# Kernel tuning notes

Hardware: AMD Instinct MI355X
Metric: run time of the kernel (lower is better)

## Reference

```python
import jax, jax.numpy as jnp
import numpy as np

B, T, D, H = 64, 1024, 128, 256

def setup_inputs() -> dict:
    key = jax.random.key(0)
    ks = jax.random.split(key, 9)
    s = 1.0 / np.sqrt(H)  # torch nn.RNN init scale
    u = lambda k, shape: jax.random.uniform(k, shape, jnp.float32, -s, s)
    return {
        "x": jax.random.normal(ks[0], (B, T, D), jnp.float32),
        "W_ih0": u(ks[1], (H, D)), "W_hh0": u(ks[2], (H, H)),
        "b_ih0": u(ks[3], (H,)),   "b_hh0": u(ks[4], (H,)),
        "W_ih1": u(ks[5], (H, H)), "W_hh1": u(ks[6], (H, H)),
        "b_ih1": u(ks[7], (H,)),   "b_hh1": u(ks[8], (H,)),
    }

def _rnn_layer(x, W_ih, W_hh, b_ih, b_hh):
    # x: [B, T, Din] -> out: [B, T, H]; h_t = tanh(x_t W_ih^T + b_ih + h_{t-1} W_hh^T + b_hh)
    xW = jnp.einsum('btd,hd->bth', x, W_ih) + b_ih  # precompute input projection
    h0 = jnp.zeros((x.shape[0], W_hh.shape[0]), x.dtype)
    def step(h, xt):
        h = jnp.tanh(xt + h @ W_hh.T + b_hh)
        return h, h
    _, ys = jax.lax.scan(step, h0, jnp.swapaxes(xW, 0, 1))  # [T, B, H]
    return jnp.swapaxes(ys, 0, 1)

def reference(x, W_ih0, W_hh0, b_ih0, b_hh0, W_ih1, W_hh1, b_ih1, b_hh1):
    h = _rnn_layer(x, W_ih0, W_hh0, b_ih0, b_hh0)
    h = _rnn_layer(h, W_ih1, W_hh1, b_ih1, b_hh1)
    return jnp.transpose(h, (0, 2, 1))  # [B, H, T] per out.permute(0, 2, 1)
```

## Files before the change

### kernel.cpp

```cpp
#include <hip/hip_runtime.h>
#include <hip/hip_bf16.h>


#define B_ 64
#define T_ 1024
#define D_ 128
#define H_ 256
#define TCMAX 128

typedef _Float16 half2_t __attribute__((ext_vector_type(2)));

__device__ __forceinline__ float bf2f(unsigned short u) {
    union { unsigned int i; float f; } v;
    v.i = ((unsigned int)u) << 16;
    return v.f;
}

__device__ __forceinline__ unsigned int cvt2_bf16_to_f16(unsigned int u) {
    union { float f; unsigned int i; } a, b;
    a.i = u << 16;
    b.i = u & 0xFFFF0000u;
    union { _Float16 h[2]; unsigned int u; } r;
    r.h[0] = (_Float16)a.f;
    r.h[1] = (_Float16)b.f;
    return r.u;
}

__device__ __forceinline__ uint4 cvt8_bf16_to_f16(uint4 v) {
    uint4 r;
    r.x = cvt2_bf16_to_f16(v.x);
    r.y = cvt2_bf16_to_f16(v.y);
    r.z = cvt2_bf16_to_f16(v.z);
    r.w = cvt2_bf16_to_f16(v.w);
    return r;
}

__device__ __forceinline__ float dot2(unsigned int a, unsigned int b, float c) {
    union { unsigned int u; half2_t h; } ua, ub;
    ua.u = a; ub.u = b;
#if defined(__HIP_DEVICE_COMPILE__) && __has_builtin(__builtin_amdgcn_fdot2)
    return __builtin_amdgcn_fdot2(ua.h, ub.h, c, false);
#else
    return c + (float)ua.h.x * (float)ub.h.x + (float)ua.h.y * (float)ub.h.y;
#endif
}

__device__ __forceinline__ float fast_tanh(float x) {
#if defined(__HIP_DEVICE_COMPILE__) && __has_builtin(__builtin_amdgcn_exp2f)
    float e = __builtin_amdgcn_exp2f(x * 2.885390081777927f);
#else
    float e = __expf(2.0f * x);
#endif
#if defined(__HIP_DEVICE_COMPILE__) && __has_builtin(__builtin_amdgcn_rcpf)
    return 1.0f - 2.0f * __builtin_amdgcn_rcpf(e + 1.0f);
#else
    return 1.0f - 2.0f / (e + 1.0f);
#endif
}

__device__ __forceinline__ void lds_barrier() {
    asm volatile("s_waitcnt lgkmcnt(0)\n\ts_barrier" ::: "memory");
}

__global__ void detect_dtype(const unsigned short* __restrict__ w, int* __restrict__ flag) {
    if (threadIdx.x == 0 && blockIdx.x == 0) {
        int f = 0;
        for (int i = 0; i < 512; ++i) {
            unsigned e = (w[i] >> 7) & 0xFF;
            if (e >= 127) f = 1;
        }
        *flag = f;
    }
}

__global__ void prep_w(const void* __restrict__ wih0, const void* __restrict__ whh0,
                       const void* __restrict__ bih0, const void* __restrict__ bhh0,
                       const void* __restrict__ wih1, const void* __restrict__ whh1,
                       const void* __restrict__ bih1, const void* __restrict__ bhh1,
                       _Float16* __restrict__ owih0, _Float16* __restrict__ owhh0,
                       _Float16* __restrict__ owih1, _Float16* __restrict__ owhh1,
                       float* __restrict__ obias0, float* __restrict__ obias1,
                       uint4* __restrict__ carries, const int* __restrict__ flag) {
    const bool f32 = (*flag != 0);
    int i = blockIdx.x * 256 + threadIdx.x;
    auto rd = [&](const void* p, int idx) -> float {
        return f32 ? ((const float*)p)[idx] : bf2f(((const unsigned short*)p)[idx]);
    };
    if (i < H_ * D_) owih0[i] = (_Float16)rd(wih0, i);
    if (i < H_ * H_) {
        owhh0[i] = (_Float16)rd(whh0, i);
        owih1[i] = (_Float16)rd(wih1, i);
        owhh1[i] = (_Float16)rd(whh1, i);
    }
    if (i < H_) {
        obias0[i] = rd(bih0, i) + rd(bhh0, i);
        obias1[i] = rd(bih1, i) + rd(bhh1, i);
    }
    if (i < (2 * B_ * H_) / 8) carries[i] = uint4{0, 0, 0, 0};
}

template <int K, bool XSRC>
__device__ __forceinline__ void proj_gemm(const void* __restrict__ src,
                                          const _Float16* __restrict__ W,
                                          const float* __restrict__ bias,
                                          _Float16* __restrict__ outx,
                                          const int* __restrict__ flag,
                                          int t0, int Tc, int pb,
                                          char* __restrict__ sm, int tid) {
    constexpr int KW = K / 8;
    const int sg = tid >> 8, j = tid & 255;
    const long m0 = (long)pb * 48;
    const bool f32 = XSRC && (*flag != 0);
    uint4* xt = (uint4*)sm;

    for (int idx = tid; idx < 48 * KW; idx += 768) {
        int r = idx / KW, c = idx % KW;
        long m = m0 + r;
        uint4 v = uint4{0, 0, 0, 0};
        if (m < (long)B_ * Tc) {
            long off;
            if (XSRC) {
                long b = m / Tc, tc = m - b * Tc;
                off = (b * T_ + t0 + tc) * (long)K + (long)c * 8;
                if (f32) {
                    const float* s = (const float*)src + off;
                    union { _Float16 h[8]; uint4 u; } r8;
#pragma unroll
                    for (int q = 0; q < 8; ++q) r8.h[q] = (_Float16)s[q];
                    v = r8.u;
                } else {
                    v = cvt8_bf16_to_f16(*(const uint4*)((const unsigned short*)src + off));
                }
            } else {
                off = m * (long)K + (long)c * 8;
                v = *(const uint4*)((const _Float16*)src + off);
            }
        }
        xt[idx] = v;
    }

    uint4 w[KW];
    const uint4* wp = (const uint4*)(W + (long)j * K);
#pragma unroll
    for (int i = 0; i < KW; ++i) w[i] = wp[i];
    __syncthreads();

    const float bb = bias[j];
#pragma unroll 1
    for (int r = 0; r < 16; ++r) {
        const long m = m0 + sg * 16 + r;
        if (m < (long)B_ * Tc) {
            const uint4* xr = xt + (sg * 16 + r) * KW;
            float a0 = 0.f, a1 = 0.f, a2 = 0.f, a3 = 0.f;
#pragma unroll
            for (int i = 0; i < KW; ++i) {
                uint4 h = xr[i];
                uint4 ww = w[i];
                a0 = dot2(ww.x, h.x, a0);
                a1 = dot2(ww.y, h.y, a1);
                a2 = dot2(ww.z, h.z, a2);
                a3 = dot2(ww.w, h.w, a3);
            }
            outx[m * H_ + j] = (_Float16)(((a0 + a1) + (a2 + a3)) + bb);
        }
    }
}

__device__ __forceinline__ void scan_layer(const _Float16* __restrict__ xw,
                                           const _Float16* __restrict__ Whh,
                                           _Float16* __restrict__ carry,
                                           _Float16* __restrict__ hout,
                                           char* __restrict__ sm, int b,
                                           int tid, int Tc) {
    __builtin_amdgcn_s_setprio(1);
    _Float16* stage = (_Float16*)sm;
    _Float16* hbuf  = (_Float16*)(sm + TCMAX * H_ * 2);
    const bool act = (tid < 512);
    const int wv = tid >> 6, lane = tid & 63, half = lane >> 5;
    const int jj = (wv & 7) * 32 + (lane & 31);

    uint4 w[16];
    if (act) {
        const uint4* wp = (const uint4*)(Whh + (long)jj * H_ + half * 128);
#pragma unroll
        for (int i = 0; i < 16; ++i) w[i] = wp[i];
    }

    {
        const uint4* src = (const uint4*)(xw + (long)b * Tc * H_);
        uint4* dst = (uint4*)stage;
        for (int i = tid; i < Tc * (H_ / 8); i += 768) dst[i] = src[i];
    }
    if (tid < 256) hbuf[tid] = carry[b * H_ + tid];
    __syncthreads();

    float hlast = 0.f;
#pragma unroll 1
    for (int it = 0; it < Tc; ++it) {
        const int p = it & 1;
        if (act) {
            float xh = (float)stage[it * H_ + jj];
            const uint4* hb = (const uint4*)(hbuf + p * H_) + half * 16;
            float a0 = 0.f, a1 = 0.f, a2 = 0.f, a3 = 0.f;
#pragma unroll
            for (int i = 0; i < 16; ++i) {
                uint4 h = hb[i];
                uint4 ww = w[i];
                a0 = dot2(ww.x, h.x, a0);
                a1 = dot2(ww.y, h.y, a1);
                a2 = dot2(ww.z, h.z, a2);
                a3 = dot2(ww.w, h.w, a3);
            }
            float s = (a0 + a1) + (a2 + a3);
            s += __shfl_xor(s, 32, 64);
            float hv = fast_tanh(s + xh);
            _Float16 hf = (_Float16)hv;
            if (half == 0) hbuf[(p ^ 1) * H_ + jj] = hf;
            else           stage[it * H_ + jj]     = hf;
            hlast = hv;
        }
        lds_barrier();
    }

    if (act && half == 0) carry[b * H_ + jj] = (_Float16)hlast;
    {
        const uint4* src = (const uint4*)stage;
        uint4* dst = (uint4*)(hout + (long)b * Tc * H_);
        for (int i = tid; i < Tc * (H_ / 8); i += 768) dst[i] = src[i];
    }
}

__device__ __forceinline__ void transpose_dev(const _Float16* __restrict__ tmp,
                                              void* __restrict__ out,
                                              const int* __restrict__ flag,
                                              int t0, int Tc, int pb,
                                              char* __restrict__ sm, int tid) {
    const int nTc = (Tc + 63) >> 6;
    int bid = pb;
    const int jblk = bid & 3; bid >>= 2;
    const int tcblk = bid % nTc;
    const int b = bid / nTc;
    const bool f32o = (*flag != 0);
    float* tile = (float*)sm;
#pragma unroll
    for (int k = 0; k < 6; ++k) {
        int idx = k * 768 + tid;
        if (idx < 4096) {
            int r = idx >> 6, c = idx & 63;
            int tc = tcblk * 64 + r;
            tile[r * 65 + c] = (tc < Tc)
                ? (float)tmp[((long)b * Tc + tc) * H_ + jblk * 64 + c] : 0.f;
        }
    }
    __syncthreads();
#pragma unroll
    for (int k = 0; k < 6; ++k) {
        int idx = k * 768 + tid;
        if (idx < 4096) {
            int jr = idx >> 6, tc = idx & 63;
            if (tcblk * 64 + tc < Tc) {
                float v = tile[tc * 65 + jr];
                long o = ((long)b * H_ + jblk * 64 + jr) * (long)T_ + t0 + tcblk * 64 + tc;
                if (f32o) ((float*)out)[o] = v;
                else      ((__hip_bfloat16*)out)[o] = __float2bfloat16(v);
            }
        }
    }
}

__global__ __launch_bounds__(768, 1) void boot(
    const void* __restrict__ x, const _Float16* __restrict__ W,
    const float* __restrict__ bias, _Float16* __restrict__ outx,
    const int* __restrict__ flag, int Tc)
{
    __shared__ __align__(16) char sm[24576];
    proj_gemm<D_, true>(x, W, bias, outx, flag, 0, Tc, blockIdx.x, sm, threadIdx.x);
}

__global__ __launch_bounds__(768, 1) void mega(
    const void* __restrict__ x,
    const _Float16* __restrict__ Wih0, const _Float16* __restrict__ Whh0,
    const _Float16* __restrict__ Wih1, const _Float16* __restrict__ Whh1,
    const float* __restrict__ bias0, const float* __restrict__ bias1,
    _Float16* __restrict__ carry0, _Float16* __restrict__ carry1,
    const _Float16* __restrict__ xw0r, _Float16* __restrict__ xw0w,
    _Float16* __restrict__ h0w, const _Float16* __restrict__ h0r,
    _Float16* __restrict__ xw1w, const _Float16* __restrict__ xw1r,
    _Float16* __restrict__ h1w, const _Float16* __restrict__ h1r,
    void* __restrict__ dout, const int* __restrict__ flag,
    int v_s0, int t_p0, int v_p1, int v_s1, int t_tr, int Tc, int nproj)
{
    __shared__ __align__(16) char sm[TCMAX * H_ * 2 + 1024];
    const int bid = blockIdx.x;
    const int tid = threadIdx.x;

    if (bid < 64) {
        if (!v_s0) return;
        scan_layer(xw0r, Whh0, carry0, h0w, sm, bid, tid, Tc);
    } else if (bid < 128) {
        if (!v_s1) return;
        scan_layer(xw1r, Whh1, carry1, h1w, sm, bid - 64, tid, Tc);
    } else if (bid < 128 + nproj) {
        if (t_p0 < 0) return;
        proj_gemm<D_, true>(x, Wih0, bias0, xw0w, flag, t_p0, Tc, bid - 128, sm, tid);
    } else if (bid < 128 + 2 * nproj) {
        if (!v_p1) return;
        proj_gemm<H_, false>(h0r, Wih1, bias1, xw1w, flag, 0, Tc, bid - 128 - nproj, sm, tid);
    } else {
        if (t_tr < 0) return;
        transpose_dev(h1r, dout, flag, t_tr, Tc, bid - 128 - 2 * nproj, sm, tid);
    }
}

extern "C" void kernel_launch(void* const* d_in, const int* in_sizes, int n_in,
                              void* d_out, int out_size, void* d_ws, size_t ws_size,
                              hipStream_t stream) {
    const void* x    = d_in[0];
    const void* wih0 = d_in[1];
    const void* whh0 = d_in[2];
    const void* bih0 = d_in[3];
    const void* bhh0 = d_in[4];
    const void* wih1 = d_in[5];
    const void* whh1 = d_in[6];
    const void* bih1 = d_in[7];
    const void* bhh1 = d_in[8];
    (void)in_sizes; (void)n_in; (void)out_size;

    char* ws = (char*)d_ws;
    size_t off = 0;
    auto alloc = [&](size_t bytes) -> void* {
        void* p = ws + off;
        off += (bytes + 255) & ~(size_t)255;
        return p;
    };

    int*      flag    = (int*)alloc(256);
    _Float16* wih0_16 = (_Float16*)alloc((size_t)H_ * D_ * 2);
    _Float16* whh0_16 = (_Float16*)alloc((size_t)H_ * H_ * 2);
    _Float16* wih1_16 = (_Float16*)alloc((size_t)H_ * H_ * 2);
    _Float16* whh1_16 = (_Float16*)alloc((size_t)H_ * H_ * 2);
    float*    bias0   = (float*)alloc(H_ * 4);
    float*    bias1   = (float*)alloc(H_ * 4);
    _Float16* carry0  = (_Float16*)alloc((size_t)B_ * H_ * 2);
    _Float16* carry1  = (_Float16*)alloc((size_t)B_ * H_ * 2);

    size_t fixed = off;
    int Tc = TCMAX;
    while (Tc > 32 && fixed + 8 * ((size_t)B_ * Tc * H_ * 2 + 256) > ws_size) Tc >>= 1;
    _Float16 *xw0g[2], *xw1g[2], *h0g[2], *h1g[2];
    for (int i = 0; i < 2; ++i) xw0g[i] = (_Float16*)alloc((size_t)B_ * Tc * H_ * 2);
    for (int i = 0; i < 2; ++i) xw1g[i] = (_Float16*)alloc((size_t)B_ * Tc * H_ * 2);
    for (int i = 0; i < 2; ++i) h0g[i]  = (_Float16*)alloc((size_t)B_ * Tc * H_ * 2);
    for (int i = 0; i < 2; ++i) h1g[i]  = (_Float16*)alloc((size_t)B_ * Tc * H_ * 2);

    detect_dtype<<<1, 64, 0, stream>>>((const unsigned short*)whh0, flag);
    prep_w<<<(H_ * H_ + 255) / 256, 256, 0, stream>>>(
        wih0, whh0, bih0, bhh0, wih1, whh1, bih1, bhh1,
        wih0_16, whh0_16, wih1_16, whh1_16, bias0, bias1, (uint4*)carry0, flag);

    const int NC     = T_ / Tc;
    const int nproj  = (B_ * Tc + 47) / 48;
    const int ntrans = B_ * ((Tc + 63) / 64) * (H_ / 64);
    const int grid   = 128 + 2 * nproj + ntrans;

    boot<<<nproj, 768, 0, stream>>>(x, wih0_16, bias0, xw0g[0], flag, Tc);

    for (int d = 0; d <= NC + 2; ++d) {
        const int v_s0 = (d < NC) ? 1 : 0;
        const int t_p0 = (d + 1 < NC) ? (d + 1) * Tc : -1;
        const int v_p1 = (d - 1 >= 0 && d - 1 < NC) ? 1 : 0;
        const int v_s1 = (d - 2 >= 0 && d - 2 < NC) ? 1 : 0;
        const int t_tr = (d - 3 >= 0 && d - 3 < NC) ? (d - 3) * Tc : -1;
        mega<<<grid, 768, 0, stream>>>(
            x, wih0_16, whh0_16, wih1_16, whh1_16, bias0, bias1,
            carry0, carry1,
            xw0g[d & 1],
            xw0g[(d + 1) & 1],
            h0g[d & 1],
            h0g[(d - 1) & 1],
            xw1g[(d - 1) & 1],
            xw1g[(d - 2) & 1],
            h1g[(d - 2) & 1],
            h1g[(d - 3) & 1],
            d_out, flag, v_s0, t_p0, v_p1, v_s1, t_tr, Tc, nproj);
    }
}
```

Before: 872.0 us.

## Compute two hidden outputs per thread with 4-way K split in RNN scan

Reworks the recurrent matvec thread mapping so that each thread computes two adjacent output units over a quarter of the K dimension, instead of one unit over half of K. Each LDS load of h is reused for two weight rows, which halves h-load traffic per FLOP. The hidden-state buffer is padded into quarter-chunks with a stride of 72 to avoid bank conflicts. The reduction now needs two cross-lane shuffle stages per output, and outputs and the carry are written as packed half pairs.

```diff
diff --git a/kernel.cpp b/kernel.cpp
--- a/kernel.cpp
+++ b/kernel.cpp
@@ -7,6 +7,7 @@
 #define D_ 128
 #define H_ 256
 #define TCMAX 128
+#define HBQ 72
 
 typedef _Float16 half2_t __attribute__((ext_vector_type(2)));
 
@@ -176,14 +177,16 @@
     _Float16* stage = (_Float16*)sm;
     _Float16* hbuf  = (_Float16*)(sm + TCMAX * H_ * 2);
     const bool act = (tid < 512);
-    const int wv = tid >> 6, lane = tid & 63, half = lane >> 5;
-    const int jj = (wv & 7) * 32 + (lane & 31);
-
-    uint4 w[16];
+    const int wv = (tid >> 6) & 7, lane = tid & 63;
+    const int kq = lane >> 4;
+    const int j0 = (wv * 16 + (lane & 15)) * 2;
+
+    uint4 w0[8], w1[8];
     if (act) {
-        const uint4* wp = (const uint4*)(Whh + (long)jj * H_ + half * 128);
-#pragma unroll
-        for (int i = 0; i < 16; ++i) w[i] = wp[i];
+        const uint4* p0 = (const uint4*)(Whh + (long)j0 * H_ + kq * 64);
+        const uint4* p1 = (const uint4*)(Whh + (long)(j0 + 1) * H_ + kq * 64);
+#pragma unroll
+        for (int i = 0; i < 8; ++i) { w0[i] = p0[i]; w1[i] = p1[i]; }
     }
 
     {
@@ -191,38 +194,43 @@
         uint4* dst = (uint4*)stage;
         for (int i = tid; i < Tc * (H_ / 8); i += 768) dst[i] = src[i];
     }
-    if (tid < 256) hbuf[tid] = carry[b * H_ + tid];
+    if (tid < 256) hbuf[(tid >> 6) * HBQ + (tid & 63)] = carry[b * H_ + tid];
     __syncthreads();
 
-    float hlast = 0.f;
+    unsigned hlast = 0;
 #pragma unroll 1
     for (int it = 0; it < Tc; ++it) {
         const int p = it & 1;
         if (act) {
-            float xh = (float)stage[it * H_ + jj];
-            const uint4* hb = (const uint4*)(hbuf + p * H_) + half * 16;
-            float a0 = 0.f, a1 = 0.f, a2 = 0.f, a3 = 0.f;
-#pragma unroll
-            for (int i = 0; i < 16; ++i) {
+            const uint4* hb = (const uint4*)(hbuf + p * (4 * HBQ) + kq * HBQ);
+            float a0 = 0.f, a1 = 0.f, b0 = 0.f, b1 = 0.f;
+#pragma unroll
+            for (int i = 0; i < 8; ++i) {
                 uint4 h = hb[i];
-                uint4 ww = w[i];
-                a0 = dot2(ww.x, h.x, a0);
-                a1 = dot2(ww.y, h.y, a1);
-                a2 = dot2(ww.z, h.z, a2);
-                a3 = dot2(ww.w, h.w, a3);
-            }
-            float s = (a0 + a1) + (a2 + a3);
-            s += __shfl_xor(s, 32, 64);
-            float hv = fast_tanh(s + xh);
-            _Float16 hf = (_Float16)hv;
-            if (half == 0) hbuf[(p ^ 1) * H_ + jj] = hf;
-            else           stage[it * H_ + jj]     = hf;
-            hlast = hv;
+                a0 = dot2(w0[i].x, h.x, a0); a1 = dot2(w0[i].y, h.y, a1);
+                b0 = dot2(w1[i].x, h.x, b0); b1 = dot2(w1[i].y, h.y, b1);
+                a0 = dot2(w0[i].z, h.z, a0); a1 = dot2(w0[i].w, h.w, a1);
+                b0 = dot2(w1[i].z, h.z, b0); b1 = dot2(w1[i].w, h.w, b1);
+            }
+            float s0 = a0 + a1, s1 = b0 + b1;
+            s0 += __shfl_xor(s0, 16, 64); s0 += __shfl_xor(s0, 32, 64);
+            s1 += __shfl_xor(s1, 16, 64); s1 += __shfl_xor(s1, 32, 64);
+            union { unsigned u; _Float16 h[2]; } xh;
+            xh.u = *(const unsigned*)(stage + it * H_ + j0);
+            union { _Float16 h[2]; unsigned u; } pk;
+            pk.h[0] = (_Float16)fast_tanh(s0 + (float)xh.h[0]);
+            pk.h[1] = (_Float16)fast_tanh(s1 + (float)xh.h[1]);
+            if (kq == 0) {
+                *(unsigned*)(hbuf + (p ^ 1) * (4 * HBQ) + (j0 >> 6) * HBQ + (j0 & 63)) = pk.u;
+            } else if (kq == 1) {
+                *(unsigned*)(stage + it * H_ + j0) = pk.u;
+            }
+            hlast = pk.u;
         }
         lds_barrier();
     }
 
-    if (act && half == 0) carry[b * H_ + jj] = (_Float16)hlast;
+    if (act && kq == 0) *(unsigned*)(carry + (long)b * H_ + j0) = hlast;
     {
         const uint4* src = (const uint4*)stage;
         uint4* dst = (uint4*)(hout + (long)b * Tc * H_);
@@ -290,7 +298,7 @@
     void* __restrict__ dout, const int* __restrict__ flag,
     int v_s0, int t_p0, int v_p1, int v_s1, int t_tr, int Tc, int nproj)
 {
-    __shared__ __align__(16) char sm[TCMAX * H_ * 2 + 1024];
+    __shared__ __align__(16) char sm[TCMAX * H_ * 2 + 2048];
     const int bid = blockIdx.x;
     const int tid = threadIdx.x;
 
```

New measurement: 941.2 us. +7.9%, slower.
